# Performance work log

Hardware: AMD Instinct MI355X
Metric: run time of the kernel (lower is better)

## Reference

```python
import jax, jax.numpy as jnp
import numpy as np

DICT = 32768
TOP_K = 128
LN_EPS = 1e-5


def setup_inputs() -> dict:
    key = jax.random.key(0)
    k_x, k_we, k_be, k_wd, k_bd = jax.random.split(key, 5)
    B, S, D = 4, 2048, 768
    x = jax.random.normal(k_x, (B, S, D), dtype=jnp.float32)
    # nn.Linear stores weight as [out, in]; init scaled roughly like orthogonal gains
    W_enc = jax.random.normal(k_we, (DICT, D), dtype=jnp.float32) / np.sqrt(D)
    b_enc = jax.random.normal(k_be, (DICT,), dtype=jnp.float32) * 0.01
    W_dec = jax.random.normal(k_wd, (D, DICT), dtype=jnp.float32) * (0.1 / np.sqrt(DICT))
    b_dec = jax.random.normal(k_bd, (D,), dtype=jnp.float32) * 0.01
    ln_gamma = jnp.ones((DICT,), dtype=jnp.float32)
    ln_beta = jnp.zeros((DICT,), dtype=jnp.float32)
    return {"x": x, "W_enc": W_enc, "b_enc": b_enc, "ln_gamma": ln_gamma,
            "ln_beta": ln_beta, "W_dec": W_dec, "b_dec": b_dec}


def _layernorm(z, gamma, beta):
    mu = jnp.mean(z, axis=-1, keepdims=True)
    var = jnp.mean(jnp.square(z - mu), axis=-1, keepdims=True)
    return (z - mu) * jax.lax.rsqrt(var + LN_EPS) * gamma + beta


def _top_k_activation(z, k):
    # keep top-k values per row, zero elsewhere (scatter, like torch.scatter_)
    vals, idx = jax.lax.top_k(z, k)            # [B,S,k]
    out = jnp.zeros_like(z)
    return jnp.put_along_axis(out, idx, vals, axis=-1, inplace=False)


def reference(x, W_enc, b_enc, ln_gamma, ln_beta, W_dec, b_dec):
    # encoder: [B,S,D] @ [D,DICT] -> [B,S,DICT]
    z = jnp.einsum("bsd,fd->bsf", x, W_enc) + b_enc
    z = _layernorm(z, ln_gamma, ln_beta)
    z = jax.nn.relu(z)
    features = _top_k_activation(z, TOP_K)      # [B,S,DICT], mostly zero
    output = jnp.einsum("bsf,df->bsd", features, W_dec) + b_dec  # [B,S,D]
    return (output, features)
```

## Files before the change

kernel.cpp:

```cpp
#include <hip/hip_runtime.h>
#include <hip/hip_bf16.h>

#define R_TOT  8192
#define DIM    768
#define FDICT  32768
#define TOPK   128
#define LN_EPS 1e-5f
#define BAND_M 0.12f
#define BAND_CAP 192

using f32x4  = __attribute__((ext_vector_type(4))) float;
using short8 = __attribute__((ext_vector_type(8))) short;

__device__ inline short f2bf(float f) {
    __hip_bfloat16 h = __float2bfloat16(f);
    return *reinterpret_cast<short*>(&h);
}
__device__ inline float bf2f(short s) {
    return __uint_as_float(((unsigned)(unsigned short)s) << 16);
}
__device__ inline void load_lds16(const void* g, void* l) {
    __builtin_amdgcn_global_load_lds(
        (const __attribute__((address_space(1))) unsigned int*)g,
        (__attribute__((address_space(3))) unsigned int*)l, 16, 0, 0);
}

__global__ __launch_bounds__(256) void conv_bf16(
    const float* __restrict__ in, unsigned short* __restrict__ out, int n8)
{
    const int i0 = blockIdx.x * 256 + threadIdx.x;
    const int stride = gridDim.x * 256;
    for (int g = i0; g < n8; g += stride) {
        const float4 a = ((const float4*)in)[g * 2];
        const float4 b = ((const float4*)in)[g * 2 + 1];
        short8 v;
        v[0] = f2bf(a.x); v[1] = f2bf(a.y); v[2] = f2bf(a.z); v[3] = f2bf(a.w);
        v[4] = f2bf(b.x); v[5] = f2bf(b.y); v[6] = f2bf(b.z); v[7] = f2bf(b.w);
        ((short8*)out)[g] = v;
    }
}

#define READ_A(P)                                                              \
    af00 = *(const short8*)&Sb[abase + (2*(P))*1024 + sw0];                    \
    af01 = *(const short8*)&Sb[abase + (2*(P))*1024 + sw1];                    \
    af10 = *(const short8*)&Sb[abase + (2*(P)+1)*1024 + sw0];                  \
    af11 = *(const short8*)&Sb[abase + (2*(P)+1)*1024 + sw1];

#define DO_MFMA(P)                                                             \
    __builtin_amdgcn_s_setprio(1);                                             \
    _Pragma("unroll")                                                          \
    for (int n = 0; n < 4; ++n) {                                              \
        acc[2*(P)][n]   = __builtin_amdgcn_mfma_f32_16x16x32_bf16(af00, bf0[n], acc[2*(P)][n],   0,0,0); \
        acc[2*(P)][n]   = __builtin_amdgcn_mfma_f32_16x16x32_bf16(af01, bf1[n], acc[2*(P)][n],   0,0,0); \
        acc[2*(P)+1][n] = __builtin_amdgcn_mfma_f32_16x16x32_bf16(af10, bf0[n], acc[2*(P)+1][n], 0,0,0); \
        acc[2*(P)+1][n] = __builtin_amdgcn_mfma_f32_16x16x32_bf16(af11, bf1[n], acc[2*(P)+1][n], 0,0,0); \
    }                                                                          \
    __builtin_amdgcn_s_setprio(0);

__global__ __launch_bounds__(512, 2) void enc_gemm(
    const unsigned short* __restrict__ Xb, const unsigned short* __restrict__ Wb,
    const float* __restrict__ benc, unsigned short* __restrict__ Zb)
{
    __shared__ __align__(16) unsigned short S[65536];

    const int t = threadIdx.x;
    const int w = t >> 6, l = t & 63;

    const int cpx = (int)gridDim.x >> 3;
    const int swz = ((int)blockIdx.x & 7) * cpx + ((int)blockIdx.x >> 3);
    const long bm = (long)(swz >> 7) * 256;
    const long bn = (long)(swz & 127) * 256;

    const int wm = w >> 2, wn = w & 3;
    const int lrow = l & 15, l4 = l >> 4;

    const int sw0 = ((l4     ) ^ (lrow & 7)) * 8;
    const int sw1 = ((4 + l4 ) ^ (lrow & 7)) * 8;
    const int abase = wm * 8192 + lrow * 64;
    const int bbase = 16384 + wn * 4096 + lrow * 64;

    const int rh0 = w * 16 + (l >> 3);
    const int rh1 = rh0 + 8;
    const int gsl = ((l & 7) ^ (l >> 3)) * 8;
    const unsigned short* pA00 = Xb + (bm +       rh0) * DIM + gsl;
    const unsigned short* pA01 = Xb + (bm +       rh1) * DIM + gsl;
    const unsigned short* pA10 = Xb + (bm + 128 + rh0) * DIM + gsl;
    const unsigned short* pA11 = Xb + (bm + 128 + rh1) * DIM + gsl;
    const unsigned short* pB00 = Wb + (bn +       rh0) * DIM + gsl;
    const unsigned short* pB01 = Wb + (bn +       rh1) * DIM + gsl;
    const unsigned short* pB10 = Wb + (bn + 128 + rh0) * DIM + gsl;
    const unsigned short* pB11 = Wb + (bn + 128 + rh1) * DIM + gsl;
    const int d00 = w * 1024;
    const int d01 = w * 1024 + 512;

    f32x4 acc[8][4];
#pragma unroll
    for (int m = 0; m < 8; ++m)
#pragma unroll
        for (int n = 0; n < 4; ++n) acc[m][n] = (f32x4){0.f, 0.f, 0.f, 0.f};

    load_lds16(pA00, S + d00);
    load_lds16(pA01, S + d01);
    load_lds16(pA10, S + 8192 + d00);
    load_lds16(pA11, S + 8192 + d01);
    load_lds16(pB00, S + 16384 + d00);
    load_lds16(pB01, S + 16384 + d01);
    load_lds16(pB10, S + 16384 + 8192 + d00);
    load_lds16(pB11, S + 16384 + 8192 + d01);
    pA00 += 64; pA01 += 64; pA10 += 64; pA11 += 64;
    pB00 += 64; pB01 += 64; pB10 += 64; pB11 += 64;

    short8 bf0[4], bf1[4];
    short8 af00, af01, af10, af11;

#pragma unroll 1
    for (int kt = 0; kt < 12; ++kt) {
        const unsigned short* Sb = S + (kt & 1) * 32768;
        unsigned short*       Sn = S + ((kt & 1) ^ 1) * 32768;

        if (kt < 11) {
            load_lds16(pA00, Sn + d00);
            load_lds16(pA01, Sn + d01);
            load_lds16(pA10, Sn + 8192 + d00);
            load_lds16(pA11, Sn + 8192 + d01);
            asm volatile("s_waitcnt vmcnt(4)" ::: "memory");
        } else {
            asm volatile("s_waitcnt vmcnt(0)" ::: "memory");
        }
        __builtin_amdgcn_s_barrier();
#pragma unroll
        for (int n = 0; n < 4; ++n) {
            bf0[n] = *(const short8*)&Sb[bbase + n * 1024 + sw0];
            bf1[n] = *(const short8*)&Sb[bbase + n * 1024 + sw1];
        }
        READ_A(0)
        DO_MFMA(0)
        asm volatile("" ::: "memory");
        __builtin_amdgcn_s_barrier();

        READ_A(1)
        if (kt < 11) {
            load_lds16(pB00, Sn + 16384 + d00);
            load_lds16(pB01, Sn + 16384 + d01);
            load_lds16(pB10, Sn + 16384 + 8192 + d00);
            load_lds16(pB11, Sn + 16384 + 8192 + d01);
        }
        asm volatile("" ::: "memory");
        __builtin_amdgcn_s_barrier();
        DO_MFMA(1)
        asm volatile("" ::: "memory");
        __builtin_amdgcn_s_barrier();

        READ_A(2)
        asm volatile("" ::: "memory");
        __builtin_amdgcn_s_barrier();
        DO_MFMA(2)
        asm volatile("" ::: "memory");
        __builtin_amdgcn_s_barrier();

        READ_A(3)
        asm volatile("" ::: "memory");
        __builtin_amdgcn_s_barrier();
        DO_MFMA(3)
        asm volatile("" ::: "memory");
        __builtin_amdgcn_s_barrier();

        pA00 += 64; pA01 += 64; pA10 += 64; pA11 += 64;
        pB00 += 64; pB01 += 64; pB10 += 64; pB11 += 64;
    }

    __syncthreads();
    float bias[4];
#pragma unroll
    for (int n = 0; n < 4; ++n) bias[n] = benc[bn + wn * 64 + n * 16 + lrow];
    unsigned short* Cs = S;
#pragma unroll
    for (int m = 0; m < 8; ++m)
#pragma unroll
        for (int n = 0; n < 4; ++n)
#pragma unroll
            for (int q = 0; q < 4; ++q)
                Cs[(wm * 128 + m * 16 + l4 * 4 + q) * 256 + wn * 64 + n * 16 + lrow] =
                    (unsigned short)f2bf(acc[m][n][q] + bias[n]);
    __syncthreads();
#pragma unroll
    for (int it = 0; it < 16; ++it) {
        const int g = t + it * 512;
        const int row = g >> 5;
        const int c8 = (g & 31) * 8;
        const short8 v = *(const short8*)&Cs[row * 256 + c8];
        __builtin_nontemporal_store(v, (short8*)&Zb[(bm + row) * FDICT + bn + c8]);
    }
}

__global__ __launch_bounds__(1024) void topk_select(
    const unsigned short* __restrict__ Zb, const float* __restrict__ gamma,
    const float* __restrict__ beta, int* __restrict__ sel_idx,
    float* __restrict__ sel_val, int* __restrict__ band_idx,
    int* __restrict__ cdef, int* __restrict__ nband,
    float* __restrict__ muarr, float* __restrict__ sinvarr,
    float* __restrict__ feat)
{
    __shared__ float    redf[32];
    __shared__ float    redm[16];
    __shared__ int      redi[2][16];
    __shared__ unsigned scomp[2];

    const int t = threadIdx.x;
    const int w = t >> 6;
    const long r = blockIdx.x;

    unsigned u[32];
    float sum = 0.f, sumsq = 0.f;
    const short8* Z8 = (const short8*)(Zb + r * (size_t)FDICT);
#pragma unroll
    for (int q = 0; q < 4; ++q) {
        const short8 v = Z8[q * 1024 + t];
#pragma unroll
        for (int j = 0; j < 8; ++j) {
            const float f = bf2f(v[j]);
            u[q * 8 + j] = __float_as_uint(f);
            sum += f; sumsq += f * f;
        }
    }
    if (t == 0) { scomp[0] = 0; scomp[1] = 0; }

    if (feat) {
        const f32x4 z4 = (f32x4){0.f, 0.f, 0.f, 0.f};
        f32x4* row4 = (f32x4*)(feat + r * (size_t)FDICT);
#pragma unroll
        for (int q = 0; q < 8; ++q)
            __builtin_nontemporal_store(z4, &row4[q * 1024 + t]);
    }

#pragma unroll
    for (int o = 32; o > 0; o >>= 1) {
        sum   += __shfl_down(sum, o, 64);
        sumsq += __shfl_down(sumsq, o, 64);
    }
    if ((t & 63) == 0) { redf[w] = sum; redf[16 + w] = sumsq; }
    __syncthreads();
    float s_ = 0.f, sq_ = 0.f;
#pragma unroll
    for (int i = 0; i < 16; ++i) { s_ += redf[i]; sq_ += redf[16 + i]; }
    const float mu = s_ / (float)FDICT;
    float var = sq_ / (float)FDICT - mu * mu;
    if (var < 0.f) var = 0.f;
    const float sinv = 1.f / sqrtf(var + LN_EPS);

    float vmax = 0.f;
#pragma unroll
    for (int q = 0; q < 4; ++q) {
        const size_t base = (size_t)(q * 1024 + t) * 8;
        const float4 g0 = *(const float4*)(gamma + base);
        const float4 g1 = *(const float4*)(gamma + base + 4);
        const float4 b0 = *(const float4*)(beta + base);
        const float4 b1 = *(const float4*)(beta + base + 4);
        const float gs[8] = {g0.x, g0.y, g0.z, g0.w, g1.x, g1.y, g1.z, g1.w};
        const float bs[8] = {b0.x, b0.y, b0.z, b0.w, b1.x, b1.y, b1.z, b1.w};
#pragma unroll
        for (int j = 0; j < 8; ++j) {
            const int i = q * 8 + j;
            const float a = fmaxf(
                fmaf((__uint_as_float(u[i]) - mu) * sinv, gs[j], bs[j]), 0.f);
            u[i] = __float_as_uint(a);
            vmax = fmaxf(vmax, a);
        }
    }
#pragma unroll
    for (int o = 32; o > 0; o >>= 1) vmax = fmaxf(vmax, __shfl_down(vmax, o, 64));
    if ((t & 63) == 0) redm[w] = vmax;
    __syncthreads();
    float m_ = 0.f;
#pragma unroll
    for (int i = 0; i < 16; ++i) m_ = fmaxf(m_, redm[i]);

    float lo = 0.f, hi = m_ + 1e-6f;
#pragma unroll 1
    for (int it = 0; it < 9; ++it) {
        const float thr = 0.5f * (lo + hi);
        int cnt = 0;
#pragma unroll
        for (int i = 0; i < 32; ++i) cnt += (__uint_as_float(u[i]) > thr);
#pragma unroll
        for (int o = 32; o > 0; o >>= 1) cnt += __shfl_down(cnt, o, 64);
        if ((t & 63) == 0) redi[it & 1][w] = cnt;
        __syncthreads();
        int stot = 0;
#pragma unroll
        for (int i = 0; i < 16; ++i) stot += redi[it & 1][i];
        if (stot >= TOPK) lo = thr; else hi = thr;
    }
    const float Tf = 0.5f * (lo + hi);
    const float thi = Tf + BAND_M, tlo = Tf - BAND_M;

#pragma unroll
    for (int i = 0; i < 32; ++i) {
        const float a = __uint_as_float(u[i]);
        const int idx = ((i >> 3) * 1024 + t) * 8 + (i & 7);
        if (a > thi) {
            const unsigned s = atomicAdd(&scomp[0], 1u);
            sel_idx[r * TOPK + s] = idx;
            sel_val[r * TOPK + s] = a;
            if (feat) feat[r * (size_t)FDICT + idx] = a;
        } else if (a >= tlo) {
            const unsigned s = atomicAdd(&scomp[1], 1u);
            if (s < BAND_CAP) band_idx[r * BAND_CAP + s] = idx;
        }
    }
    __syncthreads();
    if (t == 0) {
        cdef[r]  = (int)scomp[0];
        int nb = (int)scomp[1]; if (nb > BAND_CAP) nb = BAND_CAP;
        nband[r] = nb;
        muarr[r] = mu; sinvarr[r] = sinv;
    }
}

__global__ __launch_bounds__(256) void refine_select(
    const float* __restrict__ X, const float* __restrict__ Wenc,
    const float* __restrict__ benc, const float* __restrict__ gamma,
    const float* __restrict__ beta, const int* __restrict__ band_idx,
    const int* __restrict__ cdef, const int* __restrict__ nband,
    const float* __restrict__ muarr, const float* __restrict__ sinvarr,
    int* __restrict__ sel_idx, float* __restrict__ sel_val,
    float* __restrict__ feat)
{
    __shared__ float xs[DIM];
    __shared__ float cval[BAND_CAP];
    __shared__ int   cidx[BAND_CAP];
    __shared__ int   scnt;
    const int t = threadIdx.x;
    const long r = blockIdx.x;
    const int w = t >> 6, l = t & 63;

    for (int i = t; i < DIM; i += 256) xs[i] = X[r * DIM + i];
    if (t == 0) scnt = 0;
    const int nb = nband[r];
    const int cd = cdef[r];
    int need = TOPK - cd; if (need > nb) need = nb;
    const double mu = (double)muarr[r], sinv = (double)sinvarr[r];
    __syncthreads();

    for (int c = w; c < nb; c += 4) {
        const int fi = band_idx[r * BAND_CAP + c];
        const float* wr = Wenc + (size_t)fi * DIM;
        double s = 0.0;
        for (int k = l; k < DIM; k += 64) s = fma((double)xs[k], (double)wr[k], s);
#pragma unroll
        for (int o = 32; o > 0; o >>= 1) s += __shfl_down(s, o, 64);
        if (l == 0) {
            const double z = s + (double)benc[fi];
            const double a = (z - mu) * sinv * (double)gamma[fi] + (double)beta[fi];
            cval[c] = fmaxf((float)a, 0.f);
            cidx[c] = fi;
        }
    }
    __syncthreads();
    if (t < nb) {
        const float v = cval[t];
        const int id = cidx[t];
        int rank = 0;
        for (int j = 0; j < nb; ++j) {
            const float vj = cval[j];
            rank += (vj > v) || (vj == v && cidx[j] < id);
        }
        if (rank < need) {
            const int s = atomicAdd(&scnt, 1);
            sel_idx[r * TOPK + cd + s] = id;
            sel_val[r * TOPK + cd + s] = v;
            if (feat) feat[r * (size_t)FDICT + id] = v;
        }
    }
}

__global__ __launch_bounds__(256) void transposeWd(
    const float* __restrict__ Wd, unsigned short* __restrict__ WdTb)
{
    __shared__ float tile[32][33];
    const int fx = blockIdx.x * 32;
    const int dy = blockIdx.y * 32;
    const int tx = threadIdx.x & 31;
    const int ty = threadIdx.x >> 5;
    for (int i = ty; i < 32; i += 8)
        tile[i][tx] = Wd[(size_t)(dy + i) * FDICT + fx + tx];
    __syncthreads();
    for (int i = ty; i < 32; i += 8)
        WdTb[(size_t)(fx + i) * DIM + dy + tx] = (unsigned short)f2bf(tile[tx][i]);
}

__global__ __launch_bounds__(384) void decode(
    const int* __restrict__ sel_idx, const float* __restrict__ sel_val,
    const unsigned short* __restrict__ WdTb, const float* __restrict__ bdec,
    float* __restrict__ out)
{
    __shared__ int   sidx[TOPK];
    __shared__ float sval[TOPK];
    const int t = threadIdx.x;
    const long r = blockIdx.x;
    if (t < TOPK) { sidx[t] = sel_idx[r * TOPK + t]; sval[t] = sel_val[r * TOPK + t]; }
    __syncthreads();
    const float2 b2 = *(const float2*)(bdec + t * 2);
    float a0 = b2.x, a1 = b2.y;
    for (int j = 0; j < TOPK; ++j) {
        const unsigned wp = *(const unsigned*)(WdTb + (size_t)sidx[j] * DIM + t * 2);
        const float v = sval[j];
        a0 = fmaf(v, __uint_as_float((wp & 0xFFFFu) << 16), a0);
        a1 = fmaf(v, __uint_as_float(wp & 0xFFFF0000u), a1);
    }
    float2 o2; o2.x = a0; o2.y = a1;
    *(float2*)(out + r * DIM + t * 2) = o2;
}

__global__ __launch_bounds__(1024) void featfill(
    const int* __restrict__ sel_idx, const float* __restrict__ sel_val,
    float* __restrict__ feat)
{
    const int t = threadIdx.x;
    const long r = blockIdx.x;
    const f32x4 z4 = (f32x4){0.f, 0.f, 0.f, 0.f};
    f32x4* row4 = (f32x4*)(feat + r * FDICT);
    for (int i = t; i < FDICT / 4; i += 1024)
        __builtin_nontemporal_store(z4, &row4[i]);
    __syncthreads();
    if (t < TOPK)
        feat[r * FDICT + sel_idx[r * TOPK + t]] = sel_val[r * TOPK + t];
}

extern "C" void kernel_launch(void* const* d_in, const int* in_sizes, int n_in,
                              void* d_out, int out_size, void* d_ws, size_t ws_size,
                              hipStream_t stream)
{
    const float* x     = (const float*)d_in[0];
    const float* Wenc  = (const float*)d_in[1];
    const float* benc  = (const float*)d_in[2];
    const float* gamma = (const float*)d_in[3];
    const float* beta  = (const float*)d_in[4];
    const float* Wdec  = (const float*)d_in[5];
    const float* bdec  = (const float*)d_in[6];

    float* out  = (float*)d_out;
    float* feat = out + (size_t)R_TOT * DIM;

    unsigned short* Xb = (unsigned short*)out;

    char* ws = (char*)d_ws;
    int*   sidx  = (int*)ws;
    float* sval  = (float*)(ws + (size_t)R_TOT * TOPK * 4);
    int*   bidx  = (int*)(ws + (size_t)R_TOT * TOPK * 8);
    int*   cdef  = (int*)(ws + (size_t)R_TOT * (TOPK * 8 + BAND_CAP * 4));
    int*   nbnd  = cdef + R_TOT;
    float* muarr = (float*)(nbnd + R_TOT);
    float* sinva = muarr + R_TOT;

    const size_t WS_NEED = 624ull << 20;
    const bool big = (ws_size >= WS_NEED);

    unsigned short* Zb, *Wb, *WdTb;
    if (big) {
        Zb   = (unsigned short*)(ws + (16ull << 20));
        Wb   = (unsigned short*)(ws + (528ull << 20));
        WdTb = (unsigned short*)(ws + (576ull << 20));
    } else {
        Zb   = (unsigned short*)feat;
        Wb   = (unsigned short*)((char*)feat + 536870912ull);
        WdTb = (unsigned short*)((char*)feat + 587202560ull);
    }
    float* featArg = big ? feat : nullptr;

    conv_bf16<<<1536, 256, 0, stream>>>(x,    Xb, R_TOT * DIM / 8);
    conv_bf16<<<2048, 256, 0, stream>>>(Wenc, Wb, FDICT * DIM / 8);
    enc_gemm<<<4096, 512, 0, stream>>>(Xb, Wb, benc, Zb);
    topk_select<<<R_TOT, 1024, 0, stream>>>(Zb, gamma, beta, sidx, sval,
                                            bidx, cdef, nbnd, muarr, sinva,
                                            featArg);
    refine_select<<<R_TOT, 256, 0, stream>>>(x, Wenc, benc, gamma, beta,
                                             bidx, cdef, nbnd, muarr, sinva,
                                             sidx, sval, featArg);
    transposeWd<<<dim3(FDICT / 32, DIM / 32), 256, 0, stream>>>(Wdec, WdTb);
    decode<<<R_TOT, 384, 0, stream>>>(sidx, sval, WdTb, bdec, out);
    if (!big)
        featfill<<<R_TOT, 1024, 0, stream>>>(sidx, sval, feat);
}
```

Baseline: 1.915 ms.

## Replace 9-step bisection with 8-way histogram search and bound-derived max

Top-k threshold search drops the separate vmax reduction pass. An upper bound is derived from the row's raw min/max and a precomputed max |gamma|/|beta|. The 9 sequential bisection rounds (each a block-wide sync) become three 8-bucket counting passes using packed 16-bit counters and LDS atomics. The feature-row zero-fill moves to the end of topk_select and the scatter of definite values moves into refine_select, so zeroing is ordered before the writes. This cuts block barriers, with a looser upper bound and a small extra kernel as the cost.

```diff
diff --git a/kernel.cpp b/kernel.cpp
--- a/kernel.cpp
+++ b/kernel.cpp
@@ -37,6 +37,34 @@
         v[0] = f2bf(a.x); v[1] = f2bf(a.y); v[2] = f2bf(a.z); v[3] = f2bf(a.w);
         v[4] = f2bf(b.x); v[5] = f2bf(b.y); v[6] = f2bf(b.z); v[7] = f2bf(b.w);
         ((short8*)out)[g] = v;
+    }
+}
+
+__global__ __launch_bounds__(256) void prep_gb(
+    const float* __restrict__ gamma, const float* __restrict__ beta,
+    float* __restrict__ gbmax)
+{
+    __shared__ float rg[4], rb[4];
+    const int t = threadIdx.x;
+    float g = 0.f, b = 0.f;
+    for (int i = t; i < FDICT / 4; i += 256) {
+        const float4 g4 = ((const float4*)gamma)[i];
+        const float4 b4 = ((const float4*)beta)[i];
+        g = fmaxf(g, fmaxf(fmaxf(fabsf(g4.x), fabsf(g4.y)),
+                           fmaxf(fabsf(g4.z), fabsf(g4.w))));
+        b = fmaxf(b, fmaxf(fmaxf(fabsf(b4.x), fabsf(b4.y)),
+                           fmaxf(fabsf(b4.z), fabsf(b4.w))));
+    }
+#pragma unroll
+    for (int o = 32; o > 0; o >>= 1) {
+        g = fmaxf(g, __shfl_down(g, o, 64));
+        b = fmaxf(b, __shfl_down(b, o, 64));
+    }
+    if ((t & 63) == 0) { rg[t >> 6] = g; rb[t >> 6] = b; }
+    __syncthreads();
+    if (t == 0) {
+        gbmax[0] = fmaxf(fmaxf(rg[0], rg[1]), fmaxf(rg[2], rg[3]));
+        gbmax[1] = fmaxf(fmaxf(rb[0], rb[1]), fmaxf(rb[2], rb[3]));
     }
 }
 
@@ -195,23 +223,27 @@
 
 __global__ __launch_bounds__(1024) void topk_select(
     const unsigned short* __restrict__ Zb, const float* __restrict__ gamma,
-    const float* __restrict__ beta, int* __restrict__ sel_idx,
-    float* __restrict__ sel_val, int* __restrict__ band_idx,
-    int* __restrict__ cdef, int* __restrict__ nband,
+    const float* __restrict__ beta, const float* __restrict__ gbmax,
+    int* __restrict__ sel_idx, float* __restrict__ sel_val,
+    int* __restrict__ band_idx, int* __restrict__ cdef, int* __restrict__ nband,
     float* __restrict__ muarr, float* __restrict__ sinvarr,
     float* __restrict__ feat)
 {
-    __shared__ float    redf[32];
-    __shared__ float    redm[16];
-    __shared__ int      redi[2][16];
+    __shared__ float    redf[64];
+    __shared__ unsigned cc[12];
     __shared__ unsigned scomp[2];
 
     const int t = threadIdx.x;
     const int w = t >> 6;
     const long r = blockIdx.x;
 
+    if (t < 12) cc[t] = 0u;
+    if (t == 12) { scomp[0] = 0u; scomp[1] = 0u; }
+
+    const float gA = gbmax[0], bA = gbmax[1];
+
     unsigned u[32];
-    float sum = 0.f, sumsq = 0.f;
+    float sum = 0.f, sumsq = 0.f, zmx = -1e30f, zmn = 1e30f;
     const short8* Z8 = (const short8*)(Zb + r * (size_t)FDICT);
 #pragma unroll
     for (int q = 0; q < 4; ++q) {
@@ -221,34 +253,32 @@
             const float f = bf2f(v[j]);
             u[q * 8 + j] = __float_as_uint(f);
             sum += f; sumsq += f * f;
-        }
-    }
-    if (t == 0) { scomp[0] = 0; scomp[1] = 0; }
-
-    if (feat) {
-        const f32x4 z4 = (f32x4){0.f, 0.f, 0.f, 0.f};
-        f32x4* row4 = (f32x4*)(feat + r * (size_t)FDICT);
-#pragma unroll
-        for (int q = 0; q < 8; ++q)
-            __builtin_nontemporal_store(z4, &row4[q * 1024 + t]);
-    }
-
+            zmx = fmaxf(zmx, f); zmn = fminf(zmn, f);
+        }
+    }
 #pragma unroll
     for (int o = 32; o > 0; o >>= 1) {
         sum   += __shfl_down(sum, o, 64);
         sumsq += __shfl_down(sumsq, o, 64);
-    }
-    if ((t & 63) == 0) { redf[w] = sum; redf[16 + w] = sumsq; }
-    __syncthreads();
-    float s_ = 0.f, sq_ = 0.f;
-#pragma unroll
-    for (int i = 0; i < 16; ++i) { s_ += redf[i]; sq_ += redf[16 + i]; }
+        zmx = fmaxf(zmx, __shfl_down(zmx, o, 64));
+        zmn = fminf(zmn, __shfl_down(zmn, o, 64));
+    }
+    if ((t & 63) == 0) {
+        redf[w] = sum; redf[16 + w] = sumsq; redf[32 + w] = zmx; redf[48 + w] = zmn;
+    }
+    __syncthreads();
+    float s_ = 0.f, sq_ = 0.f, mx_ = -1e30f, mn_ = 1e30f;
+#pragma unroll
+    for (int i = 0; i < 16; ++i) {
+        s_ += redf[i]; sq_ += redf[16 + i];
+        mx_ = fmaxf(mx_, redf[32 + i]); mn_ = fminf(mn_, redf[48 + i]);
+    }
     const float mu = s_ / (float)FDICT;
     float var = sq_ / (float)FDICT - mu * mu;
     if (var < 0.f) var = 0.f;
     const float sinv = 1.f / sqrtf(var + LN_EPS);
-
-    float vmax = 0.f;
+    const float hi0 = fmaxf(mx_ - mu, mu - mn_) * sinv * gA + bA + 1e-3f;
+
 #pragma unroll
     for (int q = 0; q < 4; ++q) {
         const size_t base = (size_t)(q * 1024 + t) * 8;
@@ -261,37 +291,84 @@
 #pragma unroll
         for (int j = 0; j < 8; ++j) {
             const int i = q * 8 + j;
-            const float a = fmaxf(
-                fmaf((__uint_as_float(u[i]) - mu) * sinv, gs[j], bs[j]), 0.f);
-            u[i] = __float_as_uint(a);
-            vmax = fmaxf(vmax, a);
-        }
-    }
-#pragma unroll
-    for (int o = 32; o > 0; o >>= 1) vmax = fmaxf(vmax, __shfl_down(vmax, o, 64));
-    if ((t & 63) == 0) redm[w] = vmax;
-    __syncthreads();
-    float m_ = 0.f;
-#pragma unroll
-    for (int i = 0; i < 16; ++i) m_ = fmaxf(m_, redm[i]);
-
-    float lo = 0.f, hi = m_ + 1e-6f;
+            u[i] = __float_as_uint(fmaxf(
+                fmaf((__uint_as_float(u[i]) - mu) * sinv, gs[j], bs[j]), 0.f));
+        }
+    }
+
+    const float inv8 = 8.f / hi0;
+    int c[7];
+#pragma unroll
+    for (int j = 0; j < 7; ++j) c[j] = 0;
+#pragma unroll
+    for (int i = 0; i < 32; ++i) {
+        const float a = __uint_as_float(u[i]);
+        int b = (int)(a * inv8); b = b > 7 ? 7 : b;
+#pragma unroll
+        for (int j = 0; j < 7; ++j) c[j] += (b > j);
+    }
+    {
+        unsigned pk[4];
+        pk[0] = (unsigned)c[0] | ((unsigned)c[1] << 16);
+        pk[1] = (unsigned)c[2] | ((unsigned)c[3] << 16);
+        pk[2] = (unsigned)c[4] | ((unsigned)c[5] << 16);
+        pk[3] = (unsigned)c[6];
+#pragma unroll
+        for (int o = 32; o > 0; o >>= 1)
+#pragma unroll
+            for (int m = 0; m < 4; ++m) pk[m] += __shfl_down(pk[m], o, 64);
+        if ((t & 63) == 0)
+#pragma unroll
+            for (int m = 0; m < 4; ++m) atomicAdd(&cc[m], pk[m]);
+    }
+    __syncthreads();
+    int J = -1;
+#pragma unroll
+    for (int j = 0; j < 7; ++j) {
+        const unsigned cj = (cc[j >> 1] >> ((j & 1) * 16)) & 0xFFFFu;
+        J += (cj >= TOPK);
+    }
+    float lo = (float)(J + 1) * (hi0 * 0.125f);
+    float width = hi0 * 0.125f;
+
 #pragma unroll 1
-    for (int it = 0; it < 9; ++it) {
-        const float thr = 0.5f * (lo + hi);
-        int cnt = 0;
-#pragma unroll
-        for (int i = 0; i < 32; ++i) cnt += (__uint_as_float(u[i]) > thr);
-#pragma unroll
-        for (int o = 32; o > 0; o >>= 1) cnt += __shfl_down(cnt, o, 64);
-        if ((t & 63) == 0) redi[it & 1][w] = cnt;
+    for (int pass = 0; pass < 2; ++pass) {
+        const float st = width * 0.125f;
+        float s[7];
+#pragma unroll
+        for (int k = 0; k < 7; ++k) s[k] = lo + (float)(k + 1) * st;
+        int f[7];
+#pragma unroll
+        for (int k = 0; k < 7; ++k) f[k] = 0;
+#pragma unroll
+        for (int i = 0; i < 32; ++i) {
+            const float a = __uint_as_float(u[i]);
+#pragma unroll
+            for (int k = 0; k < 7; ++k) f[k] += (a > s[k]);
+        }
+        unsigned fp[4];
+        fp[0] = (unsigned)f[0] | ((unsigned)f[1] << 16);
+        fp[1] = (unsigned)f[2] | ((unsigned)f[3] << 16);
+        fp[2] = (unsigned)f[4] | ((unsigned)f[5] << 16);
+        fp[3] = (unsigned)f[6];
+#pragma unroll
+        for (int o = 32; o > 0; o >>= 1)
+#pragma unroll
+            for (int m = 0; m < 4; ++m) fp[m] += __shfl_down(fp[m], o, 64);
+        if ((t & 63) == 0)
+#pragma unroll
+            for (int m = 0; m < 4; ++m) atomicAdd(&cc[4 + pass * 4 + m], fp[m]);
         __syncthreads();
-        int stot = 0;
-#pragma unroll
-        for (int i = 0; i < 16; ++i) stot += redi[it & 1][i];
-        if (stot >= TOPK) lo = thr; else hi = thr;
-    }
-    const float Tf = 0.5f * (lo + hi);
+        int K = 0;
+#pragma unroll
+        for (int k = 0; k < 7; ++k) {
+            const unsigned fk = (cc[4 + pass * 4 + (k >> 1)] >> ((k & 1) * 16)) & 0xFFFFu;
+            K += (fk >= TOPK);
+        }
+        lo += (float)K * st;
+        width = st;
+    }
+    const float Tf = lo + 0.5f * width;
     const float thi = Tf + BAND_M, tlo = Tf - BAND_M;
 
 #pragma unroll
@@ -299,13 +376,12 @@
         const float a = __uint_as_float(u[i]);
         const int idx = ((i >> 3) * 1024 + t) * 8 + (i & 7);
         if (a > thi) {
-            const unsigned s = atomicAdd(&scomp[0], 1u);
-            sel_idx[r * TOPK + s] = idx;
-            sel_val[r * TOPK + s] = a;
-            if (feat) feat[r * (size_t)FDICT + idx] = a;
+            const unsigned s2 = atomicAdd(&scomp[0], 1u);
+            sel_idx[r * TOPK + s2] = idx;
+            sel_val[r * TOPK + s2] = a;
         } else if (a >= tlo) {
-            const unsigned s = atomicAdd(&scomp[1], 1u);
-            if (s < BAND_CAP) band_idx[r * BAND_CAP + s] = idx;
+            const unsigned s2 = atomicAdd(&scomp[1], 1u);
+            if (s2 < BAND_CAP) band_idx[r * BAND_CAP + s2] = idx;
         }
     }
     __syncthreads();
@@ -314,6 +390,13 @@
         int nb = (int)scomp[1]; if (nb > BAND_CAP) nb = BAND_CAP;
         nband[r] = nb;
         muarr[r] = mu; sinvarr[r] = sinv;
+    }
+    if (feat) {
+        const f32x4 z4 = (f32x4){0.f, 0.f, 0.f, 0.f};
+        f32x4* row4 = (f32x4*)(feat + r * (size_t)FDICT);
+#pragma unroll
+        for (int q = 0; q < 8; ++q)
+            __builtin_nontemporal_store(z4, &row4[q * 1024 + t]);
     }
 }
 
@@ -340,6 +423,9 @@
     const int cd = cdef[r];
     int need = TOPK - cd; if (need > nb) need = nb;
     const double mu = (double)muarr[r], sinv = (double)sinvarr[r];
+
+    if (feat && t < cd)
+        feat[r * (size_t)FDICT + sel_idx[r * TOPK + t]] = sel_val[r * TOPK + t];
     __syncthreads();
 
     for (int c = w; c < nb; c += 4) {
@@ -452,6 +538,7 @@
     int*   nbnd  = cdef + R_TOT;
     float* muarr = (float*)(nbnd + R_TOT);
     float* sinva = muarr + R_TOT;
+    float* gbmax = sinva + R_TOT;
 
     const size_t WS_NEED = 624ull << 20;
     const bool big = (ws_size >= WS_NEED);
@@ -468,12 +555,13 @@
     }
     float* featArg = big ? feat : nullptr;
 
+    prep_gb<<<1, 256, 0, stream>>>(gamma, beta, gbmax);
     conv_bf16<<<1536, 256, 0, stream>>>(x,    Xb, R_TOT * DIM / 8);
     conv_bf16<<<2048, 256, 0, stream>>>(Wenc, Wb, FDICT * DIM / 8);
     enc_gemm<<<4096, 512, 0, stream>>>(Xb, Wb, benc, Zb);
-    topk_select<<<R_TOT, 1024, 0, stream>>>(Zb, gamma, beta, sidx, sval,
-                                            bidx, cdef, nbnd, muarr, sinva,
-                                            featArg);
+    topk_select<<<R_TOT, 1024, 0, stream>>>(Zb, gamma, beta, gbmax,
+                                            sidx, sval, bidx, cdef, nbnd,
+                                            muarr, sinva, featArg);
     refine_select<<<R_TOT, 256, 0, stream>>>(x, Wenc, benc, gamma, beta,
                                              bidx, cdef, nbnd, muarr, sinva,
                                              sidx, sval, featArg);
```

New measurement: 2.074 ms. +8.3%, slower.

## Use uniform gamma/beta fast path with a predicted top-k threshold window

Applied to the files above, without the earlier changes.

Adds a one-block prep kernel that detects whether the LayerNorm gamma and beta are constant. When they are, topk_select skips the per-element gamma/beta loads, skips the max reduction, and starts the bisection from a narrow window centred on the expected Gaussian top-128 quantile (about 2.66 sigma). That takes 1 packed count pass plus 3 bisection passes instead of 9, and it falls back to a full 12-step search if the window misses. It also moves the feature-row zeroing to the end of topk_select and the scatter of the definite selections into refine_select, which adds an ordering dependency between those kernels and relies on the input distribution being near-Gaussian to get the fast path.

```diff
diff --git a/kernel.cpp b/kernel.cpp
--- a/kernel.cpp
+++ b/kernel.cpp
@@ -37,6 +37,48 @@
         v[0] = f2bf(a.x); v[1] = f2bf(a.y); v[2] = f2bf(a.z); v[3] = f2bf(a.w);
         v[4] = f2bf(b.x); v[5] = f2bf(b.y); v[6] = f2bf(b.z); v[7] = f2bf(b.w);
         ((short8*)out)[g] = v;
+    }
+}
+
+__global__ __launch_bounds__(256) void prep_gb(
+    const float* __restrict__ gamma, const float* __restrict__ beta,
+    float* __restrict__ gbinfo)
+{
+    __shared__ float rr[16];
+    const int t = threadIdx.x;
+    const int w = t >> 6;
+    float gmn = 1e30f, gmx = -1e30f, bmn = 1e30f, bmx = -1e30f;
+    for (int i = t; i < FDICT / 4; i += 256) {
+        const float4 g4 = ((const float4*)gamma)[i];
+        const float4 b4 = ((const float4*)beta)[i];
+        gmn = fminf(gmn, fminf(fminf(g4.x, g4.y), fminf(g4.z, g4.w)));
+        gmx = fmaxf(gmx, fmaxf(fmaxf(g4.x, g4.y), fmaxf(g4.z, g4.w)));
+        bmn = fminf(bmn, fminf(fminf(b4.x, b4.y), fminf(b4.z, b4.w)));
+        bmx = fmaxf(bmx, fmaxf(fmaxf(b4.x, b4.y), fmaxf(b4.z, b4.w)));
+    }
+#pragma unroll
+    for (int o = 32; o > 0; o >>= 1) {
+        gmn = fminf(gmn, __shfl_down(gmn, o, 64));
+        gmx = fmaxf(gmx, __shfl_down(gmx, o, 64));
+        bmn = fminf(bmn, __shfl_down(bmn, o, 64));
+        bmx = fmaxf(bmx, __shfl_down(bmx, o, 64));
+    }
+    if ((t & 63) == 0) {
+        rr[w * 4 + 0] = gmn; rr[w * 4 + 1] = gmx;
+        rr[w * 4 + 2] = bmn; rr[w * 4 + 3] = bmx;
+    }
+    __syncthreads();
+    if (t == 0) {
+        float a = rr[0], b = rr[1], c = rr[2], d = rr[3];
+        for (int i = 1; i < 4; ++i) {
+            a = fminf(a, rr[i * 4 + 0]); b = fmaxf(b, rr[i * 4 + 1]);
+            c = fminf(c, rr[i * 4 + 2]); d = fmaxf(d, rr[i * 4 + 3]);
+        }
+        gbinfo[0] = fmaxf(fabsf(a), fabsf(b));
+        gbinfo[1] = fmaxf(fabsf(c), fabsf(d));
+        gbinfo[2] = (a == b && c == d) ? 1.f : 0.f;
+        gbinfo[3] = b;
+        gbinfo[4] = d;
     }
 }
 
@@ -195,20 +237,22 @@
 
 __global__ __launch_bounds__(1024) void topk_select(
     const unsigned short* __restrict__ Zb, const float* __restrict__ gamma,
-    const float* __restrict__ beta, int* __restrict__ sel_idx,
-    float* __restrict__ sel_val, int* __restrict__ band_idx,
-    int* __restrict__ cdef, int* __restrict__ nband,
+    const float* __restrict__ beta, const float* __restrict__ gbinfo,
+    int* __restrict__ sel_idx, float* __restrict__ sel_val,
+    int* __restrict__ band_idx, int* __restrict__ cdef, int* __restrict__ nband,
     float* __restrict__ muarr, float* __restrict__ sinvarr,
     float* __restrict__ feat)
 {
     __shared__ float    redf[32];
-    __shared__ float    redm[16];
-    __shared__ int      redi[2][16];
+    __shared__ unsigned cacc[16];
     __shared__ unsigned scomp[2];
 
     const int t = threadIdx.x;
     const int w = t >> 6;
     const long r = blockIdx.x;
+
+    if (t < 16) cacc[t] = 0u;
+    if (t == 16) { scomp[0] = 0u; scomp[1] = 0u; }
 
     unsigned u[32];
     float sum = 0.f, sumsq = 0.f;
@@ -223,16 +267,6 @@
             sum += f; sumsq += f * f;
         }
     }
-    if (t == 0) { scomp[0] = 0; scomp[1] = 0; }
-
-    if (feat) {
-        const f32x4 z4 = (f32x4){0.f, 0.f, 0.f, 0.f};
-        f32x4* row4 = (f32x4*)(feat + r * (size_t)FDICT);
-#pragma unroll
-        for (int q = 0; q < 8; ++q)
-            __builtin_nontemporal_store(z4, &row4[q * 1024 + t]);
-    }
-
 #pragma unroll
     for (int o = 32; o > 0; o >>= 1) {
         sum   += __shfl_down(sum, o, 64);
@@ -248,50 +282,101 @@
     if (var < 0.f) var = 0.f;
     const float sinv = 1.f / sqrtf(var + LN_EPS);
 
-    float vmax = 0.f;
-#pragma unroll
-    for (int q = 0; q < 4; ++q) {
-        const size_t base = (size_t)(q * 1024 + t) * 8;
-        const float4 g0 = *(const float4*)(gamma + base);
-        const float4 g1 = *(const float4*)(gamma + base + 4);
-        const float4 b0 = *(const float4*)(beta + base);
-        const float4 b1 = *(const float4*)(beta + base + 4);
-        const float gs[8] = {g0.x, g0.y, g0.z, g0.w, g1.x, g1.y, g1.z, g1.w};
-        const float bs[8] = {b0.x, b0.y, b0.z, b0.w, b1.x, b1.y, b1.z, b1.w};
-#pragma unroll
-        for (int j = 0; j < 8; ++j) {
-            const int i = q * 8 + j;
-            const float a = fmaxf(
-                fmaf((__uint_as_float(u[i]) - mu) * sinv, gs[j], bs[j]), 0.f);
-            u[i] = __float_as_uint(a);
-            vmax = fmaxf(vmax, a);
-        }
-    }
-#pragma unroll
-    for (int o = 32; o > 0; o >>= 1) vmax = fmaxf(vmax, __shfl_down(vmax, o, 64));
-    if ((t & 63) == 0) redm[w] = vmax;
-    __syncthreads();
-    float m_ = 0.f;
-#pragma unroll
-    for (int i = 0; i < 16; ++i) m_ = fmaxf(m_, redm[i]);
-
-    float lo = 0.f, hi = m_ + 1e-6f;
+    const float g0 = gbinfo[3], b0 = gbinfo[4];
+    const bool uniform = (gbinfo[2] != 0.f) && (g0 > 0.f) && (g0 <= 2.f);
+
+    if (uniform) {
+        const float gs = sinv * g0;
+#pragma unroll
+        for (int i = 0; i < 32; ++i)
+            u[i] = __float_as_uint(fmaxf(
+                fmaf(__uint_as_float(u[i]) - mu, gs, b0), 0.f));
+    } else {
+#pragma unroll
+        for (int q = 0; q < 4; ++q) {
+            const size_t base = (size_t)(q * 1024 + t) * 8;
+            const float4 g4a = *(const float4*)(gamma + base);
+            const float4 g4b = *(const float4*)(gamma + base + 4);
+            const float4 b4a = *(const float4*)(beta + base);
+            const float4 b4b = *(const float4*)(beta + base + 4);
+            const float gs[8] = {g4a.x, g4a.y, g4a.z, g4a.w, g4b.x, g4b.y, g4b.z, g4b.w};
+            const float bs[8] = {b4a.x, b4a.y, b4a.z, b4a.w, b4b.x, b4b.y, b4b.z, b4b.w};
+#pragma unroll
+            for (int j = 0; j < 8; ++j) {
+                const int i = q * 8 + j;
+                u[i] = __float_as_uint(fmaxf(
+                    fmaf((__uint_as_float(u[i]) - mu) * sinv, gs[j], bs[j]), 0.f));
+            }
+        }
+    }
+
+    float Tf = 0.f;
+    bool got = false;
+    int nextacc = 0;
+    if (uniform) {
+        const float Vh = fmaf(2.6601f, g0, b0);
+        const float h  = 0.25f * g0;
+        float lo = Vh - h, hi = Vh + h;
+        unsigned pc = 0;
+#pragma unroll
+        for (int i = 0; i < 32; ++i) {
+            const float a = __uint_as_float(u[i]);
+            pc += (a > lo) ? 1u : 0u;
+            pc += (a > hi) ? 0x10000u : 0u;
+        }
+#pragma unroll
+        for (int o = 32; o > 0; o >>= 1) pc += __shfl_down(pc, o, 64);
+        if ((t & 63) == 0) atomicAdd(&cacc[0], pc);
+        __syncthreads();
+        const unsigned clo = cacc[0] & 0xFFFFu, chi = cacc[0] >> 16;
+        if (clo >= TOPK && chi < TOPK) {
 #pragma unroll 1
-    for (int it = 0; it < 9; ++it) {
-        const float thr = 0.5f * (lo + hi);
-        int cnt = 0;
-#pragma unroll
-        for (int i = 0; i < 32; ++i) cnt += (__uint_as_float(u[i]) > thr);
-#pragma unroll
-        for (int o = 32; o > 0; o >>= 1) cnt += __shfl_down(cnt, o, 64);
-        if ((t & 63) == 0) redi[it & 1][w] = cnt;
+            for (int it = 1; it <= 3; ++it) {
+                const float thr = 0.5f * (lo + hi);
+                unsigned cnt = 0;
+#pragma unroll
+                for (int i = 0; i < 32; ++i)
+                    cnt += (__uint_as_float(u[i]) > thr) ? 1u : 0u;
+#pragma unroll
+                for (int o = 32; o > 0; o >>= 1) cnt += __shfl_down(cnt, o, 64);
+                if ((t & 63) == 0) atomicAdd(&cacc[it], cnt);
+                __syncthreads();
+                if (cacc[it] >= TOPK) lo = thr; else hi = thr;
+            }
+            Tf = 0.5f * (lo + hi);
+            got = true;
+        }
+        nextacc = 4;
+    }
+    if (!got) {
         __syncthreads();
-        int stot = 0;
-#pragma unroll
-        for (int i = 0; i < 16; ++i) stot += redi[it & 1][i];
-        if (stot >= TOPK) lo = thr; else hi = thr;
-    }
-    const float Tf = 0.5f * (lo + hi);
+        float vmax = 0.f;
+#pragma unroll
+        for (int i = 0; i < 32; ++i) vmax = fmaxf(vmax, __uint_as_float(u[i]));
+#pragma unroll
+        for (int o = 32; o > 0; o >>= 1) vmax = fmaxf(vmax, __shfl_down(vmax, o, 64));
+        if ((t & 63) == 0) redf[w] = vmax;
+        __syncthreads();
+        float mx = 0.f;
+#pragma unroll
+        for (int i = 0; i < 16; ++i) mx = fmaxf(mx, redf[i]);
+        float lo = 0.f, hi = mx + 1e-6f;
+#pragma unroll 1
+        for (int it = 0; it < 12; ++it) {
+            const float thr = 0.5f * (lo + hi);
+            unsigned cnt = 0;
+#pragma unroll
+            for (int i = 0; i < 32; ++i)
+                cnt += (__uint_as_float(u[i]) > thr) ? 1u : 0u;
+#pragma unroll
+            for (int o = 32; o > 0; o >>= 1) cnt += __shfl_down(cnt, o, 64);
+            if ((t & 63) == 0) atomicAdd(&cacc[nextacc + it], cnt);
+            __syncthreads();
+            if (cacc[nextacc + it] >= TOPK) lo = thr; else hi = thr;
+        }
+        Tf = 0.5f * (lo + hi);
+    }
+
     const float thi = Tf + BAND_M, tlo = Tf - BAND_M;
 
 #pragma unroll
@@ -299,13 +384,12 @@
         const float a = __uint_as_float(u[i]);
         const int idx = ((i >> 3) * 1024 + t) * 8 + (i & 7);
         if (a > thi) {
-            const unsigned s = atomicAdd(&scomp[0], 1u);
-            sel_idx[r * TOPK + s] = idx;
-            sel_val[r * TOPK + s] = a;
-            if (feat) feat[r * (size_t)FDICT + idx] = a;
+            const unsigned s2 = atomicAdd(&scomp[0], 1u);
+            sel_idx[r * TOPK + s2] = idx;
+            sel_val[r * TOPK + s2] = a;
         } else if (a >= tlo) {
-            const unsigned s = atomicAdd(&scomp[1], 1u);
-            if (s < BAND_CAP) band_idx[r * BAND_CAP + s] = idx;
+            const unsigned s2 = atomicAdd(&scomp[1], 1u);
+            if (s2 < BAND_CAP) band_idx[r * BAND_CAP + s2] = idx;
         }
     }
     __syncthreads();
@@ -314,6 +398,13 @@
         int nb = (int)scomp[1]; if (nb > BAND_CAP) nb = BAND_CAP;
         nband[r] = nb;
         muarr[r] = mu; sinvarr[r] = sinv;
+    }
+    if (feat) {
+        const f32x4 z4 = (f32x4){0.f, 0.f, 0.f, 0.f};
+        f32x4* row4 = (f32x4*)(feat + r * (size_t)FDICT);
+#pragma unroll
+        for (int q = 0; q < 8; ++q)
+            __builtin_nontemporal_store(z4, &row4[q * 1024 + t]);
     }
 }
 
@@ -340,6 +431,9 @@
     const int cd = cdef[r];
     int need = TOPK - cd; if (need > nb) need = nb;
     const double mu = (double)muarr[r], sinv = (double)sinvarr[r];
+
+    if (feat && t < cd)
+        feat[r * (size_t)FDICT + sel_idx[r * TOPK + t]] = sel_val[r * TOPK + t];
     __syncthreads();
 
     for (int c = w; c < nb; c += 4) {
@@ -452,6 +546,7 @@
     int*   nbnd  = cdef + R_TOT;
     float* muarr = (float*)(nbnd + R_TOT);
     float* sinva = muarr + R_TOT;
+    float* gbinfo = sinva + R_TOT;
 
     const size_t WS_NEED = 624ull << 20;
     const bool big = (ws_size >= WS_NEED);
@@ -468,12 +563,13 @@
     }
     float* featArg = big ? feat : nullptr;
 
+    prep_gb<<<1, 256, 0, stream>>>(gamma, beta, gbinfo);
     conv_bf16<<<1536, 256, 0, stream>>>(x,    Xb, R_TOT * DIM / 8);
     conv_bf16<<<2048, 256, 0, stream>>>(Wenc, Wb, FDICT * DIM / 8);
     enc_gemm<<<4096, 512, 0, stream>>>(Xb, Wb, benc, Zb);
-    topk_select<<<R_TOT, 1024, 0, stream>>>(Zb, gamma, beta, sidx, sval,
-                                            bidx, cdef, nbnd, muarr, sinva,
-                                            featArg);
+    topk_select<<<R_TOT, 1024, 0, stream>>>(Zb, gamma, beta, gbinfo,
+                                            sidx, sval, bidx, cdef, nbnd,
+                                            muarr, sinva, featArg);
     refine_select<<<R_TOT, 256, 0, stream>>>(x, Wenc, benc, gamma, beta,
                                              bidx, cdef, nbnd, muarr, sinva,
                                              sidx, sval, featArg);
```

Result: faster. 1.790 ms (-6.5%).
